# Kernel optimization log

Hardware: AMD Instinct MI355X
Metric: run time of the kernel (lower is better)

The kernel has to match this reference:

```python
import jax, jax.numpy as jnp
import numpy as np

B, N, C = 2, 3136, 256
NUM_HEADS = 8
RADIUS = 3.0


def spatial_mask(H, W, radius):
    # [N, 2] pixel coordinates, then pairwise Euclidean distance mask
    yy, xx = jnp.meshgrid(jnp.arange(H), jnp.arange(W), indexing='ij')
    coords = jnp.stack([yy, xx], axis=-1).astype(jnp.float32).reshape(-1, 2)
    d2 = jnp.sum((coords[:, None, :] - coords[None, :, :]) ** 2, axis=-1)
    return jnp.where(d2 > radius * radius, -jnp.inf, 0.0)  # [N, N]


def setup_inputs() -> dict:
    key = jax.random.key(0)
    ks = jax.random.split(key, 7)
    w = 0.02
    return {
        'x': jax.random.normal(ks[0], (B, N, C), jnp.float32),
        'x_kv': jax.random.normal(ks[1], (B, N, C), jnp.float32),
        'Wq': jax.random.normal(ks[2], (C, C), jnp.float32) * w,
        'Wk': jax.random.normal(ks[3], (C, C), jnp.float32) * w,
        'Wv': jax.random.normal(ks[4], (C, C), jnp.float32) * w,
        'Wp': jax.random.normal(ks[5], (C, C), jnp.float32) * w,
        'bp': jnp.zeros((C,), jnp.float32),
    }


def reference(x, x_kv, Wq, Wk, Wv, Wp, bp):
    Bc, Nc, Cc = x.shape
    H = W = int(Nc ** 0.5)
    hd = Cc // NUM_HEADS
    scale = hd ** (-0.5)
    # torch Linear: y = x @ W.T ; split heads -> [B, h, N, hd]
    q = (x @ Wq.T).reshape(Bc, Nc, NUM_HEADS, hd).transpose(0, 2, 1, 3)
    k = (x_kv @ Wk.T).reshape(Bc, Nc, NUM_HEADS, hd).transpose(0, 2, 1, 3)
    v = (x_kv @ Wv.T).reshape(Bc, Nc, NUM_HEADS, hd).transpose(0, 2, 1, 3)
    attn = jnp.einsum('bhnd,bhmd->bhnm', q, k) * scale
    attn = attn + spatial_mask(H, W, RADIUS)[None, None, :, :]
    attn = jax.nn.softmax(attn, axis=-1)
    out = jnp.einsum('bhnm,bhmd->bhnd', attn, v)
    out = out.transpose(0, 2, 1, 3).reshape(Bc, Nc, Cc)
    return out @ Wp.T + bp
```

## Files before the change

kernel.cpp:

```cpp
#include <hip/hip_runtime.h>


typedef float  f32x4  __attribute__((ext_vector_type(4)));
typedef __bf16 bf16x8 __attribute__((ext_vector_type(8)));
typedef unsigned short u16x4 __attribute__((ext_vector_type(4)));
typedef unsigned short u16x8 __attribute__((ext_vector_type(8)));

#define Bb    2
#define Nn    3136
#define Cc    256
#define Mrows (Bb * Nn)
#define BNC   (Bb * Nn * Cc)
#define CC    (Cc * Cc)
#define GRID56 56

__device__ __forceinline__ unsigned short f2bf(float f) {
    unsigned u = __builtin_bit_cast(unsigned, f);
    u += 0x7fffu + ((u >> 16) & 1u);
    return (unsigned short)(u >> 16);
}

__global__ __launch_bounds__(256) void convert_all(
    const float* __restrict__ x,  const float* __restrict__ xkv,
    const float* __restrict__ wq, const float* __restrict__ wk,
    const float* __restrict__ wv, const float* __restrict__ wp,
    unsigned short* __restrict__ xb,  unsigned short* __restrict__ xkvb,
    unsigned short* __restrict__ wqb, unsigned short* __restrict__ wkb,
    unsigned short* __restrict__ wvb, unsigned short* __restrict__ wpb)
{
    const int NX = BNC / 4;
    const int NW = CC / 4;
    int i = blockIdx.x * blockDim.x + threadIdx.x;
    const float* src; unsigned short* dst; int off;
    if (i < NX)            { src = x;   dst = xb;   off = i; }
    else if (i < 2 * NX)   { src = xkv; dst = xkvb; off = i - NX; }
    else {
        int j = i - 2 * NX;
        int wsel = j / NW; off = j - wsel * NW;
        src = (wsel == 0) ? wq : (wsel == 1) ? wk : (wsel == 2) ? wv : wp;
        dst = (wsel == 0) ? wqb : (wsel == 1) ? wkb : (wsel == 2) ? wvb : wpb;
    }
    f32x4 v = *reinterpret_cast<const f32x4*>(src + (size_t)off * 4);
    u16x4 o;
    o[0] = f2bf(v[0]); o[1] = f2bf(v[1]); o[2] = f2bf(v[2]); o[3] = f2bf(v[3]);
    *reinterpret_cast<u16x4*>(dst + (size_t)off * 4) = o;
}

template<bool BIAS>
__device__ __forceinline__ void gemm_body(
    const unsigned short* __restrict__ A,
    const unsigned short* __restrict__ W,
    const float* __restrict__ bias,
    float* __restrict__ Y,
    int m0, int n0)
{
    constexpr int K = 256;
    constexpr int LDSW = 40;
    __shared__ unsigned short lA[64 * LDSW];
    __shared__ unsigned short lB[64 * LDSW];

    const int t    = threadIdx.x;
    const int lane = t & 63;
    const int wave = t >> 6;
    const int wm   = wave >> 1;
    const int wn   = wave & 1;
    const int srow = t >> 2;
    const int sseg = t & 3;
    const int fr   = lane & 15;
    const int fk   = (lane >> 4) * 8;

    f32x4 acc[2][2] = {};

    for (int k0 = 0; k0 < K; k0 += 32) {
        u16x8 av = *reinterpret_cast<const u16x8*>(A + (size_t)(m0 + srow) * K + k0 + sseg * 8);
        u16x8 bv = *reinterpret_cast<const u16x8*>(W + (size_t)(n0 + srow) * K + k0 + sseg * 8);
        __syncthreads();
        *reinterpret_cast<u16x8*>(&lA[srow * LDSW + sseg * 8]) = av;
        *reinterpret_cast<u16x8*>(&lB[srow * LDSW + sseg * 8]) = bv;
        __syncthreads();

        bf16x8 af[2], bfr[2];
#pragma unroll
        for (int i = 0; i < 2; ++i) {
            af[i]  = *reinterpret_cast<const bf16x8*>(&lA[(wm * 32 + i * 16 + fr) * LDSW + fk]);
            bfr[i] = *reinterpret_cast<const bf16x8*>(&lB[(wn * 32 + i * 16 + fr) * LDSW + fk]);
        }
#pragma unroll
        for (int i = 0; i < 2; ++i)
#pragma unroll
            for (int j = 0; j < 2; ++j)
                acc[i][j] = __builtin_amdgcn_mfma_f32_16x16x32_bf16(af[i], bfr[j], acc[i][j], 0, 0, 0);
    }

#pragma unroll
    for (int i = 0; i < 2; ++i)
#pragma unroll
        for (int j = 0; j < 2; ++j) {
            int rbase = m0 + wm * 32 + i * 16 + (lane >> 4) * 4;
            int c     = n0 + wn * 32 + j * 16 + (lane & 15);
            float badd = BIAS ? bias[c] : 0.0f;
#pragma unroll
            for (int e = 0; e < 4; ++e)
                Y[(size_t)(rbase + e) * 256 + c] = acc[i][j][e] + badd;
        }
}

__global__ __launch_bounds__(256) void gemm_qkv_kernel(
    const unsigned short* __restrict__ xb, const unsigned short* __restrict__ xkvb,
    const unsigned short* __restrict__ wqb, const unsigned short* __restrict__ wkb,
    const unsigned short* __restrict__ wvb,
    float* __restrict__ Q, float* __restrict__ Kf, float* __restrict__ Vf)
{
    int z = blockIdx.z;
    const unsigned short* A = (z == 0) ? xb : xkvb;
    const unsigned short* W = (z == 0) ? wqb : (z == 1 ? wkb : wvb);
    float* Y = (z == 0) ? Q : (z == 1 ? Kf : Vf);
    gemm_body<false>(A, W, nullptr, Y, blockIdx.x * 64, blockIdx.y * 64);
}

__global__ __launch_bounds__(256) void gemm_proj_kernel(
    const unsigned short* __restrict__ Ab, const unsigned short* __restrict__ wpb,
    const float* __restrict__ bias, float* __restrict__ Y)
{
    gemm_body<true>(Ab, wpb, bias, Y, blockIdx.x * 64, blockIdx.y * 64);
}

__global__ __launch_bounds__(256) void attn_local(
    const float* __restrict__ Q, const float* __restrict__ K,
    const float* __restrict__ V, unsigned short* __restrict__ outb)
{
    const int wave = threadIdx.x >> 6;
    const int lane = threadIdx.x & 63;
    const int q = blockIdx.x * 4 + wave;
    const int b = q / Nn;
    const int n = q - b * Nn;
    const int y = n / GRID56;
    const int x = n - y * GRID56;
    const float scale = 0.17677669529663687f;

    f32x4 qv = *reinterpret_cast<const f32x4*>(Q + (size_t)q * Cc + lane * 4);

    float m_run = -INFINITY, l_run = 0.0f;
    f32x4 acc = {0.0f, 0.0f, 0.0f, 0.0f};

#pragma unroll
    for (int dy = -3; dy <= 3; ++dy) {
        int yy = y + dy;
        if ((unsigned)yy >= (unsigned)GRID56) continue;
        int R = (dy == 0) ? 3 : ((dy == 3 || dy == -3) ? 0 : 2);
#pragma unroll
        for (int dx = -3; dx <= 3; ++dx) {
            if (dx < -R || dx > R) continue;
            int xx = x + dx;
            if ((unsigned)xx >= (unsigned)GRID56) continue;
            int m = b * Nn + yy * GRID56 + xx;
            f32x4 kv = *reinterpret_cast<const f32x4*>(K + (size_t)m * Cc + lane * 4);
            float p = qv[0] * kv[0] + qv[1] * kv[1] + qv[2] * kv[2] + qv[3] * kv[3];
            p += __shfl_xor(p, 1);
            p += __shfl_xor(p, 2);
            p += __shfl_xor(p, 4);
            float s = p * scale;
            float m_new = fmaxf(m_run, s);
            float corr = __expf(m_run - m_new);
            float pe   = __expf(s - m_new);
            l_run = l_run * corr + pe;
            f32x4 vv = *reinterpret_cast<const f32x4*>(V + (size_t)m * Cc + lane * 4);
            acc[0] = acc[0] * corr + pe * vv[0];
            acc[1] = acc[1] * corr + pe * vv[1];
            acc[2] = acc[2] * corr + pe * vv[2];
            acc[3] = acc[3] * corr + pe * vv[3];
            m_run = m_new;
        }
    }
    float inv = 1.0f / l_run;
    u16x4 o;
    o[0] = f2bf(acc[0] * inv); o[1] = f2bf(acc[1] * inv);
    o[2] = f2bf(acc[2] * inv); o[3] = f2bf(acc[3] * inv);
    *reinterpret_cast<u16x4*>(outb + (size_t)q * Cc + lane * 4) = o;
}

extern "C" void kernel_launch(void* const* d_in, const int* in_sizes, int n_in,
                              void* d_out, int out_size, void* d_ws, size_t ws_size,
                              hipStream_t stream)
{
    const float* x   = (const float*)d_in[0];
    const float* xkv = (const float*)d_in[1];
    const float* Wq  = (const float*)d_in[2];
    const float* Wk  = (const float*)d_in[3];
    const float* Wv  = (const float*)d_in[4];
    const float* Wp  = (const float*)d_in[5];
    const float* bp  = (const float*)d_in[6];
    float* out = (float*)d_out;

    char* ws = (char*)d_ws;
    unsigned short* xb   = (unsigned short*)ws; ws += (size_t)BNC * 2;
    unsigned short* xkvb = (unsigned short*)ws; ws += (size_t)BNC * 2;
    unsigned short* wqb  = (unsigned short*)ws; ws += (size_t)CC * 2;
    unsigned short* wkb  = (unsigned short*)ws; ws += (size_t)CC * 2;
    unsigned short* wvb  = (unsigned short*)ws; ws += (size_t)CC * 2;
    unsigned short* wpb  = (unsigned short*)ws; ws += (size_t)CC * 2;
    float* Qf = (float*)ws; ws += (size_t)BNC * 4;
    float* Kf = (float*)ws; ws += (size_t)BNC * 4;
    float* Vf = (float*)ws; ws += (size_t)BNC * 4;
    unsigned short* attb = (unsigned short*)ws; ws += (size_t)BNC * 2;

    convert_all<<<3392, 256, 0, stream>>>(x, xkv, Wq, Wk, Wv, Wp,
                                          xb, xkvb, wqb, wkb, wvb, wpb);
    dim3 gqkv(Mrows / 64, Cc / 64, 3);
    gemm_qkv_kernel<<<gqkv, 256, 0, stream>>>(xb, xkvb, wqb, wkb, wvb, Qf, Kf, Vf);
    attn_local<<<Mrows / 4, 256, 0, stream>>>(Qf, Kf, Vf, attb);
    dim3 gproj(Mrows / 64, Cc / 64, 1);
    gemm_proj_kernel<<<gproj, 256, 0, stream>>>(attb, wpb, bp, out);
}
```

Baseline: 115.7 us.

## Fuse fp32-to-bf16 conversion into GEMM loads and store Q/K/V as bf16

Removes the separate conversion kernel by converting fp32 activations and weights to bf16 inside the GEMM tile loads, and widens the K step to 64. The QKV GEMM now writes bf16 Q/K/V, halving intermediate traffic for the attention kernel, which decodes bf16 on load. This trades a launch and a round trip through memory for repeated weight conversion in every block, plus extra rounding of Q/K/V before attention.

```diff
diff --git a/kernel.cpp b/kernel.cpp
--- a/kernel.cpp
+++ b/kernel.cpp
@@ -6,12 +6,10 @@
 typedef unsigned short u16x4 __attribute__((ext_vector_type(4)));
 typedef unsigned short u16x8 __attribute__((ext_vector_type(8)));
 
-#define Bb    2
 #define Nn    3136
 #define Cc    256
-#define Mrows (Bb * Nn)
-#define BNC   (Bb * Nn * Cc)
-#define CC    (Cc * Cc)
+#define Mrows 6272
+#define BNC   1605632
 #define GRID56 56
 
 __device__ __forceinline__ unsigned short f2bf(float f) {
@@ -19,43 +17,18 @@
     u += 0x7fffu + ((u >> 16) & 1u);
     return (unsigned short)(u >> 16);
 }
-
-__global__ __launch_bounds__(256) void convert_all(
-    const float* __restrict__ x,  const float* __restrict__ xkv,
-    const float* __restrict__ wq, const float* __restrict__ wk,
-    const float* __restrict__ wv, const float* __restrict__ wp,
-    unsigned short* __restrict__ xb,  unsigned short* __restrict__ xkvb,
-    unsigned short* __restrict__ wqb, unsigned short* __restrict__ wkb,
-    unsigned short* __restrict__ wvb, unsigned short* __restrict__ wpb)
-{
-    const int NX = BNC / 4;
-    const int NW = CC / 4;
-    int i = blockIdx.x * blockDim.x + threadIdx.x;
-    const float* src; unsigned short* dst; int off;
-    if (i < NX)            { src = x;   dst = xb;   off = i; }
-    else if (i < 2 * NX)   { src = xkv; dst = xkvb; off = i - NX; }
-    else {
-        int j = i - 2 * NX;
-        int wsel = j / NW; off = j - wsel * NW;
-        src = (wsel == 0) ? wq : (wsel == 1) ? wk : (wsel == 2) ? wv : wp;
-        dst = (wsel == 0) ? wqb : (wsel == 1) ? wkb : (wsel == 2) ? wvb : wpb;
-    }
-    f32x4 v = *reinterpret_cast<const f32x4*>(src + (size_t)off * 4);
-    u16x4 o;
-    o[0] = f2bf(v[0]); o[1] = f2bf(v[1]); o[2] = f2bf(v[2]); o[3] = f2bf(v[3]);
-    *reinterpret_cast<u16x4*>(dst + (size_t)off * 4) = o;
-}
-
-template<bool BIAS>
+__device__ __forceinline__ float bf2f(unsigned short h) {
+    unsigned u = (unsigned)h << 16;
+    return __builtin_bit_cast(float, u);
+}
+
+template<bool A_BF16, bool OUT_BF16>
 __device__ __forceinline__ void gemm_body(
-    const unsigned short* __restrict__ A,
-    const unsigned short* __restrict__ W,
-    const float* __restrict__ bias,
-    float* __restrict__ Y,
+    const void* __restrict__ Ap, const float* __restrict__ W,
+    const float* __restrict__ bias, void* __restrict__ Yv,
     int m0, int n0)
 {
-    constexpr int K = 256;
-    constexpr int LDSW = 40;
+    constexpr int LDSW = 72;
     __shared__ unsigned short lA[64 * LDSW];
     __shared__ unsigned short lB[64 * LDSW];
 
@@ -65,31 +38,64 @@
     const int wm   = wave >> 1;
     const int wn   = wave & 1;
     const int srow = t >> 2;
-    const int sseg = t & 3;
+    const int scol = (t & 3) * 16;
     const int fr   = lane & 15;
     const int fk   = (lane >> 4) * 8;
 
     f32x4 acc[2][2] = {};
 
-    for (int k0 = 0; k0 < K; k0 += 32) {
-        u16x8 av = *reinterpret_cast<const u16x8*>(A + (size_t)(m0 + srow) * K + k0 + sseg * 8);
-        u16x8 bv = *reinterpret_cast<const u16x8*>(W + (size_t)(n0 + srow) * K + k0 + sseg * 8);
+    for (int k0 = 0; k0 < 256; k0 += 64) {
+        u16x8 astage[2], bstage[2];
+        if constexpr (A_BF16) {
+            const unsigned short* A = (const unsigned short*)Ap;
+            astage[0] = *reinterpret_cast<const u16x8*>(A + (size_t)(m0 + srow) * 256 + k0 + scol);
+            astage[1] = *reinterpret_cast<const u16x8*>(A + (size_t)(m0 + srow) * 256 + k0 + scol + 8);
+        } else {
+            const float* A = (const float*)Ap;
+            f32x4 a4[4];
+#pragma unroll
+            for (int j = 0; j < 4; ++j)
+                a4[j] = *reinterpret_cast<const f32x4*>(A + (size_t)(m0 + srow) * 256 + k0 + scol + j * 4);
+#pragma unroll
+            for (int j = 0; j < 4; ++j)
+#pragma unroll
+                for (int e = 0; e < 4; ++e)
+                    astage[j >> 1][(j & 1) * 4 + e] = f2bf(a4[j][e]);
+        }
+        {
+            f32x4 b4[4];
+#pragma unroll
+            for (int j = 0; j < 4; ++j)
+                b4[j] = *reinterpret_cast<const f32x4*>(W + (size_t)(n0 + srow) * 256 + k0 + scol + j * 4);
+#pragma unroll
+            for (int j = 0; j < 4; ++j)
+#pragma unroll
+                for (int e = 0; e < 4; ++e)
+                    bstage[j >> 1][(j & 1) * 4 + e] = f2bf(b4[j][e]);
+        }
+
         __syncthreads();
-        *reinterpret_cast<u16x8*>(&lA[srow * LDSW + sseg * 8]) = av;
-        *reinterpret_cast<u16x8*>(&lB[srow * LDSW + sseg * 8]) = bv;
+        *reinterpret_cast<u16x8*>(&lA[srow * LDSW + scol])     = astage[0];
+        *reinterpret_cast<u16x8*>(&lA[srow * LDSW + scol + 8]) = astage[1];
+        *reinterpret_cast<u16x8*>(&lB[srow * LDSW + scol])     = bstage[0];
+        *reinterpret_cast<u16x8*>(&lB[srow * LDSW + scol + 8]) = bstage[1];
         __syncthreads();
 
-        bf16x8 af[2], bfr[2];
-#pragma unroll
-        for (int i = 0; i < 2; ++i) {
-            af[i]  = *reinterpret_cast<const bf16x8*>(&lA[(wm * 32 + i * 16 + fr) * LDSW + fk]);
-            bfr[i] = *reinterpret_cast<const bf16x8*>(&lB[(wn * 32 + i * 16 + fr) * LDSW + fk]);
-        }
+        bf16x8 af[2][2], bfr[2][2];
 #pragma unroll
         for (int i = 0; i < 2; ++i)
 #pragma unroll
-            for (int j = 0; j < 2; ++j)
-                acc[i][j] = __builtin_amdgcn_mfma_f32_16x16x32_bf16(af[i], bfr[j], acc[i][j], 0, 0, 0);
+            for (int h = 0; h < 2; ++h) {
+                af[i][h]  = *reinterpret_cast<const bf16x8*>(&lA[(wm * 32 + i * 16 + fr) * LDSW + h * 32 + fk]);
+                bfr[i][h] = *reinterpret_cast<const bf16x8*>(&lB[(wn * 32 + i * 16 + fr) * LDSW + h * 32 + fk]);
+            }
+#pragma unroll
+        for (int h = 0; h < 2; ++h)
+#pragma unroll
+            for (int i = 0; i < 2; ++i)
+#pragma unroll
+                for (int j = 0; j < 2; ++j)
+                    acc[i][j] = __builtin_amdgcn_mfma_f32_16x16x32_bf16(af[i][h], bfr[j][h], acc[i][j], 0, 0, 0);
     }
 
 #pragma unroll
@@ -97,37 +103,46 @@
 #pragma unroll
         for (int j = 0; j < 2; ++j) {
             int rbase = m0 + wm * 32 + i * 16 + (lane >> 4) * 4;
-            int c     = n0 + wn * 32 + j * 16 + (lane & 15);
-            float badd = BIAS ? bias[c] : 0.0f;
-#pragma unroll
-            for (int e = 0; e < 4; ++e)
-                Y[(size_t)(rbase + e) * 256 + c] = acc[i][j][e] + badd;
+            int c     = n0 + wn * 32 + j * 16 + fr;
+            if constexpr (OUT_BF16) {
+                unsigned short* Y = (unsigned short*)Yv;
+#pragma unroll
+                for (int e = 0; e < 4; ++e)
+                    Y[(size_t)(rbase + e) * 256 + c] = f2bf(acc[i][j][e]);
+            } else {
+                float* Y = (float*)Yv;
+                float badd = bias[c];
+#pragma unroll
+                for (int e = 0; e < 4; ++e)
+                    Y[(size_t)(rbase + e) * 256 + c] = acc[i][j][e] + badd;
+            }
         }
 }
 
 __global__ __launch_bounds__(256) void gemm_qkv_kernel(
-    const unsigned short* __restrict__ xb, const unsigned short* __restrict__ xkvb,
-    const unsigned short* __restrict__ wqb, const unsigned short* __restrict__ wkb,
-    const unsigned short* __restrict__ wvb,
-    float* __restrict__ Q, float* __restrict__ Kf, float* __restrict__ Vf)
+    const float* __restrict__ x, const float* __restrict__ xkv,
+    const float* __restrict__ Wq, const float* __restrict__ Wk,
+    const float* __restrict__ Wv,
+    unsigned short* __restrict__ Qb, unsigned short* __restrict__ Kb,
+    unsigned short* __restrict__ Vb)
 {
     int z = blockIdx.z;
-    const unsigned short* A = (z == 0) ? xb : xkvb;
-    const unsigned short* W = (z == 0) ? wqb : (z == 1 ? wkb : wvb);
-    float* Y = (z == 0) ? Q : (z == 1 ? Kf : Vf);
-    gemm_body<false>(A, W, nullptr, Y, blockIdx.x * 64, blockIdx.y * 64);
+    const float* A = (z == 0) ? x : xkv;
+    const float* W = (z == 0) ? Wq : (z == 1 ? Wk : Wv);
+    unsigned short* Y = (z == 0) ? Qb : (z == 1 ? Kb : Vb);
+    gemm_body<false, true>(A, W, nullptr, Y, blockIdx.x * 64, blockIdx.y * 64);
 }
 
 __global__ __launch_bounds__(256) void gemm_proj_kernel(
-    const unsigned short* __restrict__ Ab, const unsigned short* __restrict__ wpb,
+    const unsigned short* __restrict__ attb, const float* __restrict__ Wp,
     const float* __restrict__ bias, float* __restrict__ Y)
 {
-    gemm_body<true>(Ab, wpb, bias, Y, blockIdx.x * 64, blockIdx.y * 64);
+    gemm_body<true, false>(attb, Wp, bias, Y, blockIdx.x * 64, blockIdx.y * 64);
 }
 
 __global__ __launch_bounds__(256) void attn_local(
-    const float* __restrict__ Q, const float* __restrict__ K,
-    const float* __restrict__ V, unsigned short* __restrict__ outb)
+    const unsigned short* __restrict__ Q, const unsigned short* __restrict__ K,
+    const unsigned short* __restrict__ V, unsigned short* __restrict__ outb)
 {
     const int wave = threadIdx.x >> 6;
     const int lane = threadIdx.x & 63;
@@ -138,7 +153,8 @@
     const int x = n - y * GRID56;
     const float scale = 0.17677669529663687f;
 
-    f32x4 qv = *reinterpret_cast<const f32x4*>(Q + (size_t)q * Cc + lane * 4);
+    u16x4 qr = *reinterpret_cast<const u16x4*>(Q + (size_t)q * Cc + lane * 4);
+    float q0 = bf2f(qr[0]), q1 = bf2f(qr[1]), q2 = bf2f(qr[2]), q3 = bf2f(qr[3]);
 
     float m_run = -INFINITY, l_run = 0.0f;
     f32x4 acc = {0.0f, 0.0f, 0.0f, 0.0f};
@@ -154,8 +170,9 @@
             int xx = x + dx;
             if ((unsigned)xx >= (unsigned)GRID56) continue;
             int m = b * Nn + yy * GRID56 + xx;
-            f32x4 kv = *reinterpret_cast<const f32x4*>(K + (size_t)m * Cc + lane * 4);
-            float p = qv[0] * kv[0] + qv[1] * kv[1] + qv[2] * kv[2] + qv[3] * kv[3];
+            u16x4 kr = *reinterpret_cast<const u16x4*>(K + (size_t)m * Cc + lane * 4);
+            u16x4 vr = *reinterpret_cast<const u16x4*>(V + (size_t)m * Cc + lane * 4);
+            float p = q0 * bf2f(kr[0]) + q1 * bf2f(kr[1]) + q2 * bf2f(kr[2]) + q3 * bf2f(kr[3]);
             p += __shfl_xor(p, 1);
             p += __shfl_xor(p, 2);
             p += __shfl_xor(p, 4);
@@ -164,11 +181,10 @@
             float corr = __expf(m_run - m_new);
             float pe   = __expf(s - m_new);
             l_run = l_run * corr + pe;
-            f32x4 vv = *reinterpret_cast<const f32x4*>(V + (size_t)m * Cc + lane * 4);
-            acc[0] = acc[0] * corr + pe * vv[0];
-            acc[1] = acc[1] * corr + pe * vv[1];
-            acc[2] = acc[2] * corr + pe * vv[2];
-            acc[3] = acc[3] * corr + pe * vv[3];
+            acc[0] = acc[0] * corr + pe * bf2f(vr[0]);
+            acc[1] = acc[1] * corr + pe * bf2f(vr[1]);
+            acc[2] = acc[2] * corr + pe * bf2f(vr[2]);
+            acc[3] = acc[3] * corr + pe * bf2f(vr[3]);
             m_run = m_new;
         }
     }
@@ -193,22 +209,14 @@
     float* out = (float*)d_out;
 
     char* ws = (char*)d_ws;
-    unsigned short* xb   = (unsigned short*)ws; ws += (size_t)BNC * 2;
-    unsigned short* xkvb = (unsigned short*)ws; ws += (size_t)BNC * 2;
-    unsigned short* wqb  = (unsigned short*)ws; ws += (size_t)CC * 2;
-    unsigned short* wkb  = (unsigned short*)ws; ws += (size_t)CC * 2;
-    unsigned short* wvb  = (unsigned short*)ws; ws += (size_t)CC * 2;
-    unsigned short* wpb  = (unsigned short*)ws; ws += (size_t)CC * 2;
-    float* Qf = (float*)ws; ws += (size_t)BNC * 4;
-    float* Kf = (float*)ws; ws += (size_t)BNC * 4;
-    float* Vf = (float*)ws; ws += (size_t)BNC * 4;
+    unsigned short* Qb   = (unsigned short*)ws; ws += (size_t)BNC * 2;
+    unsigned short* Kb   = (unsigned short*)ws; ws += (size_t)BNC * 2;
+    unsigned short* Vb   = (unsigned short*)ws; ws += (size_t)BNC * 2;
     unsigned short* attb = (unsigned short*)ws; ws += (size_t)BNC * 2;
 
-    convert_all<<<3392, 256, 0, stream>>>(x, xkv, Wq, Wk, Wv, Wp,
-                                          xb, xkvb, wqb, wkb, wvb, wpb);
     dim3 gqkv(Mrows / 64, Cc / 64, 3);
-    gemm_qkv_kernel<<<gqkv, 256, 0, stream>>>(xb, xkvb, wqb, wkb, wvb, Qf, Kf, Vf);
-    attn_local<<<Mrows / 4, 256, 0, stream>>>(Qf, Kf, Vf, attb);
+    gemm_qkv_kernel<<<gqkv, 256, 0, stream>>>(x, xkv, Wq, Wk, Wv, Qb, Kb, Vb);
+    attn_local<<<Mrows / 4, 256, 0, stream>>>(Qb, Kb, Vb, attb);
     dim3 gproj(Mrows / 64, Cc / 64, 1);
-    gemm_proj_kernel<<<gproj, 256, 0, stream>>>(attb, wpb, bp, out);
-}
+    gemm_proj_kernel<<<gproj, 256, 0, stream>>>(attb, Wp, bp, out);
+}
```

Result: no change. 115.6 us (-0.1%).
